# Performance work log

Hardware: AMD Instinct MI355X
Metric: run time of the kernel (lower is better)

## Reference

```python
import jax, jax.numpy as jnp
import numpy as np

N = 100000
E = 1600000
C_IN = 64
C_OUT = 64
EPS = 1e-12  # torch F.normalize default eps


def setup_inputs() -> dict:
    key = jax.random.key(0)
    k1, k2, k3, k4 = jax.random.split(key, 4)
    x = jax.random.normal(k1, (N, C_IN), dtype=jnp.float32)
    edge_index = jax.random.randint(k2, (2, E), 0, N, dtype=jnp.int64)
    # Linear(2*in_channels -> out_channels): W [out, 2*in], b [out]
    W = jax.random.normal(k3, (C_OUT, 2 * C_IN), dtype=jnp.float32) * (1.0 / np.sqrt(2 * C_IN))
    b = jax.random.normal(k4, (C_OUT,), dtype=jnp.float32) * 0.01
    return {"x": x, "edge_index": edge_index, "W": W, "b": b, "num_nodes": N}


def reference(x, edge_index, W, b, num_nodes):
    src = edge_index[0]
    dst = edge_index[1]
    # gather messages from source nodes, mean-aggregate per destination (CSC semantics)
    msg = x[src]                                   # [E, C_in]
    agg = jax.ops.segment_sum(msg, dst, num_segments=num_nodes)          # [N, C_in]
    deg = jax.ops.segment_sum(jnp.ones((msg.shape[0],), dtype=x.dtype), dst,
                              num_segments=num_nodes)                    # [N]
    agg = agg / jnp.maximum(deg, 1.0)[:, None]     # mean; zero-degree nodes -> 0
    # SAGEConvAgg output layout: concat([aggregated, root]) -> [N, 2*C_in]
    h = jnp.concatenate([agg, x], axis=-1)
    out = h @ W.T + b                              # [N, C_out]
    # l2 normalize (F.normalize, p=2, dim=-1)
    norm = jnp.sqrt(jnp.sum(out * out, axis=-1, keepdims=True))
    out = out / jnp.maximum(norm, EPS)
    return out
```

## Files before the change

### kernel.cpp

```cpp
#include <hip/hip_runtime.h>
#include <math.h>

#define CIN 64
#define NB_MAX 1024
#define CAP 2560
#define EPB 4096
#define B1T 256

__device__ __forceinline__ float rdlane_f(float v, int l) {
    return __uint_as_float(__builtin_amdgcn_readlane(__float_as_uint(v), l));
}
__device__ __forceinline__ int rdlane_i(int v, int l) {
    return (int)__builtin_amdgcn_readlane((unsigned)v, l);
}

__global__ __launch_bounds__(B1T) void build_kernel(const int* __restrict__ src,
                                                    const int* __restrict__ dst,
                                                    int* __restrict__ gcur,
                                                    int* __restrict__ coarse,
                                                    int E, int NB) {
    __shared__ int hist[NB_MAX];
    __shared__ int base[NB_MAX];
    __shared__ int cur[NB_MAX];
    const int t = threadIdx.x;
    for (int i = t; i < NB; i += B1T) { hist[i] = 0; cur[i] = 0; }
    __syncthreads();
    const int e0 = blockIdx.x * EPB;
#pragma unroll
    for (int k = 0; k < EPB / B1T; ++k) {
        int e = e0 + t + k * B1T;
        if (e < E) atomicAdd(&hist[((unsigned)dst[e]) >> 7], 1);
    }
    __syncthreads();
    for (int i = t; i < NB; i += B1T)
        base[i] = hist[i] ? atomicAdd(&gcur[i], hist[i]) : 0;
    __syncthreads();
#pragma unroll
    for (int k = 0; k < EPB / B1T; ++k) {
        int e = e0 + t + k * B1T;
        if (e < E) {
            int d  = dst[e];
            int bk = ((unsigned)d) >> 7;
            int pos = base[bk] + atomicAdd(&cur[bk], 1);
            if (pos < CAP)
                coarse[(size_t)bk * CAP + pos] = ((d & 127) << 17) | src[e];
        }
    }
}

__global__ __launch_bounds__(256) void csr_kernel(const int* __restrict__ gcur,
                                                  int* __restrict__ coarse,
                                                  int2* __restrict__ meta, int N) {
    __shared__ int pk[CAP];
    __shared__ int cnt[128], off[128], cur[128];
    const int t = threadIdx.x;
    const int bkt = blockIdx.x;
    const int m0 = gcur[bkt];
    const int m = (m0 < CAP) ? m0 : CAP;

    for (int i = t; i < m; i += 256) pk[i] = coarse[(size_t)bkt * CAP + i];
    if (t < 128) { cnt[t] = 0; cur[t] = 0; }
    __syncthreads();

    for (int i = t; i < m; i += 256) atomicAdd(&cnt[((unsigned)pk[i]) >> 17], 1);
    __syncthreads();

    int v = 0;
    if (t < 128) { v = cnt[t]; off[t] = v; }
    __syncthreads();
    for (int d = 1; d < 128; d <<= 1) {
        int add = 0;
        if (t < 128 && t >= d) add = off[t - d];
        __syncthreads();
        if (t < 128) off[t] += add;
        __syncthreads();
    }
    if (t < 128) off[t] -= v;
    __syncthreads();

    for (int i = t; i < m; i += 256) {
        int p = pk[i];
        int d = ((unsigned)p) >> 17;
        int pos = atomicAdd(&cur[d], 1);
        coarse[(size_t)bkt * CAP + off[d] + pos] = p & 0x1FFFF;
    }
    if (t < 128) {
        int n = bkt * 128 + t;
        if (n < N) meta[n] = make_int2(bkt * CAP + off[t], cnt[t]);
    }
}

__global__ __launch_bounds__(256) void gather_mean_kernel(
        const float* __restrict__ x, const int2* __restrict__ meta,
        const int* __restrict__ csr, float* __restrict__ agg, int N) {
    const int lane = threadIdx.x & 63;
    const int half = lane >> 5;
    const int c2   = lane & 31;

    const int wid = blockIdx.x * 4 + (threadIdx.x >> 6);
    const int nw  = gridDim.x * 4;

    for (int n = wid; n < N; n += nw) {
        const int2 mt = meta[n];
        const int o   = __builtin_amdgcn_readfirstlane(mt.x);
        const int deg = __builtin_amdgcn_readfirstlane(mt.y);
        const int md  = (deg < 64) ? deg : 64;

        int sv = (lane < md) ? csr[o + lane] : 0;

        float2 p0 = make_float2(0.f, 0.f), p1 = make_float2(0.f, 0.f);
        float2 p2 = make_float2(0.f, 0.f), p3 = make_float2(0.f, 0.f);
        int j = 0;
        for (; j + 8 <= md; j += 8) {
            int sA0 = rdlane_i(sv, j + 0), sB0 = rdlane_i(sv, j + 1);
            int sA1 = rdlane_i(sv, j + 2), sB1 = rdlane_i(sv, j + 3);
            int sA2 = rdlane_i(sv, j + 4), sB2 = rdlane_i(sv, j + 5);
            int sA3 = rdlane_i(sv, j + 6), sB3 = rdlane_i(sv, j + 7);
            int s0 = half ? sB0 : sA0;
            int s1 = half ? sB1 : sA1;
            int s2 = half ? sB2 : sA2;
            int s3 = half ? sB3 : sA3;
            const float2 v0 = *(const float2*)(x + ((size_t)s0 << 6) + (c2 << 1));
            const float2 v1 = *(const float2*)(x + ((size_t)s1 << 6) + (c2 << 1));
            const float2 v2 = *(const float2*)(x + ((size_t)s2 << 6) + (c2 << 1));
            const float2 v3 = *(const float2*)(x + ((size_t)s3 << 6) + (c2 << 1));
            p0.x += v0.x; p0.y += v0.y;
            p1.x += v1.x; p1.y += v1.y;
            p2.x += v2.x; p2.y += v2.y;
            p3.x += v3.x; p3.y += v3.y;
        }
        for (; j + 2 <= md; j += 2) {
            int sA = rdlane_i(sv, j), sB = rdlane_i(sv, j + 1);
            int s = half ? sB : sA;
            const float2 v = *(const float2*)(x + ((size_t)s << 6) + (c2 << 1));
            p0.x += v.x; p0.y += v.y;
        }
        if (j < md) {
            int s = rdlane_i(sv, j);
            if (half == 0) {
                const float2 v = *(const float2*)(x + ((size_t)s << 6) + (c2 << 1));
                p0.x += v.x; p0.y += v.y;
            }
        }
        float hx = (p0.x + p1.x) + (p2.x + p3.x);
        float hy = (p0.y + p1.y) + (p2.y + p3.y);
        hx += __shfl_xor(hx, 32, 64);
        hy += __shfl_xor(hy, 32, 64);
        const float inv = 1.0f / fmaxf((float)deg, 1.0f);
        if (half == 0)
            *(float2*)(agg + ((size_t)n << 6) + (c2 << 1)) =
                make_float2(hx * inv, hy * inv);
    }
}

__global__ __launch_bounds__(256) void linear_norm_kernel(
        const float* __restrict__ x, const float* __restrict__ agg,
        const float* __restrict__ W, const float* __restrict__ b,
        float* __restrict__ out, int N) {
    const int lane = threadIdx.x & 63;
    const int c2   = lane & 31;
    const float bias = b[lane];

    const int wid = blockIdx.x * 4 + (threadIdx.x >> 6);
    const int nw  = gridDim.x * 4;

    for (int n = wid; n < N; n += nw) {
        const float2 h  = *(const float2*)(agg + ((size_t)n << 6) + (c2 << 1));
        const float root = x[((size_t)n << 6) + lane];

        float c0 = bias, c1 = 0.f, c2a = 0.f, c3a = 0.f;
#pragma unroll
        for (int q = 0; q < 16; ++q) {
            const float4 wq = *(const float4*)(W + lane * 2 * CIN + q * 4);
            c0  = fmaf(rdlane_f(h.x, 2 * q),     wq.x, c0);
            c1  = fmaf(rdlane_f(h.y, 2 * q),     wq.y, c1);
            c2a = fmaf(rdlane_f(h.x, 2 * q + 1), wq.z, c2a);
            c3a = fmaf(rdlane_f(h.y, 2 * q + 1), wq.w, c3a);
        }
#pragma unroll
        for (int q = 0; q < 16; ++q) {
            const float4 wq = *(const float4*)(W + lane * 2 * CIN + CIN + q * 4);
            c0  = fmaf(rdlane_f(root, 4 * q + 0), wq.x, c0);
            c1  = fmaf(rdlane_f(root, 4 * q + 1), wq.y, c1);
            c2a = fmaf(rdlane_f(root, 4 * q + 2), wq.z, c2a);
            c3a = fmaf(rdlane_f(root, 4 * q + 3), wq.w, c3a);
        }
        float acc = (c0 + c1) + (c2a + c3a);

        float sq = acc * acc;
#pragma unroll
        for (int offs = 32; offs > 0; offs >>= 1)
            sq += __shfl_xor(sq, offs, 64);
        out[(size_t)n * CIN + lane] = acc / fmaxf(sqrtf(sq), 1e-12f);
    }
}

extern "C" void kernel_launch(void* const* d_in, const int* in_sizes, int n_in,
                              void* d_out, int out_size, void* d_ws, size_t ws_size,
                              hipStream_t stream) {
    const float* x  = (const float*)d_in[0];
    const int*   ei = (const int*)d_in[1];
    const float* W  = (const float*)d_in[2];
    const float* b  = (const float*)d_in[3];

    const int N = in_sizes[0] / CIN;
    const int E = in_sizes[1] / 2;
    const int* src = ei;
    const int* dst = ei + E;

    const int NB = (N + 127) >> 7;

    int2*  meta   = (int2*)d_ws;
    int*   gcur   = (int*)(meta + ((N + 1) & ~1));
    int*   coarse = gcur + NB_MAX;
    float* agg    = (float*)(coarse + (size_t)NB_MAX * CAP);

    hipMemsetAsync(gcur, 0, (size_t)NB * sizeof(int), stream);

    const int blocks1 = (E + EPB - 1) / EPB;
    build_kernel<<<blocks1, B1T, 0, stream>>>(src, dst, gcur, coarse, E, NB);

    csr_kernel<<<NB, 256, 0, stream>>>(gcur, coarse, meta, N);

    gather_mean_kernel<<<4096, 256, 0, stream>>>(x, meta, coarse, agg, N);

    linear_norm_kernel<<<2048, 256, 0, stream>>>(x, agg, W, b,
                                                 (float*)d_out, N);
}
```

Baseline: 261.8 us.

## Keep W rows in registers and broadcast node features through LDS

The linear+normalize kernel now loads each lane's full 128-element W row into registers once, instead of reloading it from memory for every node. Per-node agg and x values are staged in a per-wave LDS buffer and read back as float4 broadcasts, replacing the readlane broadcasts. The next node's features are prefetched while the current one is computed. The grid shrinks to 512 blocks with launch_bounds(256,2) to fit the large register footprint, which limits occupancy.

```diff
diff --git a/kernel.cpp b/kernel.cpp
--- a/kernel.cpp
+++ b/kernel.cpp
@@ -153,45 +153,61 @@
     }
 }
 
-__global__ __launch_bounds__(256) void linear_norm_kernel(
+__global__ __launch_bounds__(256, 2) void linear_norm_kernel(
         const float* __restrict__ x, const float* __restrict__ agg,
         const float* __restrict__ W, const float* __restrict__ b,
         float* __restrict__ out, int N) {
+    __shared__ __align__(16) float hbuf[4][128];
     const int lane = threadIdx.x & 63;
-    const int c2   = lane & 31;
+    const int wv   = threadIdx.x >> 6;
     const float bias = b[lane];
 
-    const int wid = blockIdx.x * 4 + (threadIdx.x >> 6);
+    float4 w[32];
+#pragma unroll
+    for (int q = 0; q < 32; ++q)
+        w[q] = *(const float4*)(W + lane * 2 * CIN + q * 4);
+#pragma unroll
+    for (int q = 0; q < 32; ++q)
+        asm volatile("" : "+v"(w[q].x), "+v"(w[q].y), "+v"(w[q].z), "+v"(w[q].w));
+
+    const int wid = blockIdx.x * 4 + wv;
     const int nw  = gridDim.x * 4;
-
-    for (int n = wid; n < N; n += nw) {
-        const float2 h  = *(const float2*)(agg + ((size_t)n << 6) + (c2 << 1));
-        const float root = x[((size_t)n << 6) + lane];
-
-        float c0 = bias, c1 = 0.f, c2a = 0.f, c3a = 0.f;
-#pragma unroll
-        for (int q = 0; q < 16; ++q) {
-            const float4 wq = *(const float4*)(W + lane * 2 * CIN + q * 4);
-            c0  = fmaf(rdlane_f(h.x, 2 * q),     wq.x, c0);
-            c1  = fmaf(rdlane_f(h.y, 2 * q),     wq.y, c1);
-            c2a = fmaf(rdlane_f(h.x, 2 * q + 1), wq.z, c2a);
-            c3a = fmaf(rdlane_f(h.y, 2 * q + 1), wq.w, c3a);
-        }
-#pragma unroll
-        for (int q = 0; q < 16; ++q) {
-            const float4 wq = *(const float4*)(W + lane * 2 * CIN + CIN + q * 4);
-            c0  = fmaf(rdlane_f(root, 4 * q + 0), wq.x, c0);
-            c1  = fmaf(rdlane_f(root, 4 * q + 1), wq.y, c1);
-            c2a = fmaf(rdlane_f(root, 4 * q + 2), wq.z, c2a);
-            c3a = fmaf(rdlane_f(root, 4 * q + 3), wq.w, c3a);
-        }
-        float acc = (c0 + c1) + (c2a + c3a);
+    const float4* hb = (const float4*)hbuf[wv];
+
+    int n = wid;
+    float av = 0.f, xv = 0.f;
+    if (n < N) {
+        av = agg[((size_t)n << 6) + lane];
+        xv = x[((size_t)n << 6) + lane];
+    }
+    for (; n < N; n += nw) {
+        hbuf[wv][lane]      = av;
+        hbuf[wv][64 + lane] = xv;
+        const int n2 = n + nw;
+        if (n2 < N) {
+            av = agg[((size_t)n2 << 6) + lane];
+            xv = x[((size_t)n2 << 6) + lane];
+        }
+        __builtin_amdgcn_wave_barrier();
+
+        float c0 = bias, c1 = 0.f, c2v = 0.f, c3v = 0.f;
+#pragma unroll
+        for (int q = 0; q < 32; ++q) {
+            const float4 hq = hb[q];
+            c0  = fmaf(hq.x, w[q].x, c0);
+            c1  = fmaf(hq.y, w[q].y, c1);
+            c2v = fmaf(hq.z, w[q].z, c2v);
+            c3v = fmaf(hq.w, w[q].w, c3v);
+        }
+        float acc = (c0 + c1) + (c2v + c3v);
 
         float sq = acc * acc;
 #pragma unroll
         for (int offs = 32; offs > 0; offs >>= 1)
             sq += __shfl_xor(sq, offs, 64);
         out[(size_t)n * CIN + lane] = acc / fmaxf(sqrtf(sq), 1e-12f);
+
+        __builtin_amdgcn_wave_barrier();
     }
 }
 
@@ -224,6 +240,6 @@
 
     gather_mean_kernel<<<4096, 256, 0, stream>>>(x, meta, coarse, agg, N);
 
-    linear_norm_kernel<<<2048, 256, 0, stream>>>(x, agg, W, b,
-                                                 (float*)d_out, N);
-}
+    linear_norm_kernel<<<512, 256, 0, stream>>>(x, agg, W, b,
+                                                (float*)d_out, N);
+}
```

New measurement: 251.8 us. -3.8%, faster.

## Restructure linear+normalize kernel to per-thread nodes with W staged in LDS

Applied to the files above, without the earlier changes.

The linear/normalize kernel now assigns two nodes per thread and accumulates all 64 outputs in registers, reading W from shared memory via broadcast. This replaces the per-wave readlane-based matvec and the cross-lane reduction for the norm. The aim is fewer cross-lane ops and better FMA density. The cost is very high register use, one block per CU, and strided per-thread global loads of agg and x rows.

```diff
diff --git a/kernel.cpp b/kernel.cpp
--- a/kernel.cpp
+++ b/kernel.cpp
@@ -153,45 +153,123 @@
     }
 }
 
-__global__ __launch_bounds__(256) void linear_norm_kernel(
+__global__ __launch_bounds__(256, 1) void linear_norm_kernel(
         const float* __restrict__ x, const float* __restrict__ agg,
         const float* __restrict__ W, const float* __restrict__ b,
         float* __restrict__ out, int N) {
+    __shared__ __align__(16) float w_lds[64 * 128 + 64];
+
+    {
+        const float4* Wv = (const float4*)W;
+        float4* w4s = (float4*)w_lds;
+        for (int i = threadIdx.x; i < 2048; i += 256) w4s[i] = Wv[i];
+        if (threadIdx.x < 16)
+            ((float4*)(w_lds + 8192))[threadIdx.x] = ((const float4*)b)[threadIdx.x];
+    }
+    __syncthreads();
+
     const int lane = threadIdx.x & 63;
-    const int c2   = lane & 31;
-    const float bias = b[lane];
-
-    const int wid = blockIdx.x * 4 + (threadIdx.x >> 6);
-    const int nw  = gridDim.x * 4;
-
-    for (int n = wid; n < N; n += nw) {
-        const float2 h  = *(const float2*)(agg + ((size_t)n << 6) + (c2 << 1));
-        const float root = x[((size_t)n << 6) + lane];
-
-        float c0 = bias, c1 = 0.f, c2a = 0.f, c3a = 0.f;
+    const int wv   = threadIdx.x >> 6;
+    const int n0   = (blockIdx.x * 4 + wv) * 128;
+    const int nA   = n0 + lane;
+    const int nB   = n0 + 64 + lane;
+    const int nAs  = (nA < N) ? nA : (N - 1);
+    const int nBs  = (nB < N) ? nB : (N - 1);
+
+    const float4* w4 = (const float4*)w_lds;
+    const float4* b4 = (const float4*)(w_lds + 8192);
+    const float4* ha = (const float4*)agg;
+    const float4* hx = (const float4*)x;
+
+    float accA[64], accB[64];
+#pragma unroll
+    for (int q = 0; q < 16; ++q) {
+        const float4 bq = b4[q];
+        accA[4 * q + 0] = bq.x; accB[4 * q + 0] = bq.x;
+        accA[4 * q + 1] = bq.y; accB[4 * q + 1] = bq.y;
+        accA[4 * q + 2] = bq.z; accB[4 * q + 2] = bq.z;
+        accA[4 * q + 3] = bq.w; accB[4 * q + 3] = bq.w;
+    }
+
+    float4 hA = ha[((size_t)nAs << 4)];
+    float4 hB = ha[((size_t)nBs << 4)];
+    for (int kq = 0; kq < 16; ++kq) {
+        const float4 cA = hA, cB = hB;
+        if (kq < 15) {
+            hA = ha[((size_t)nAs << 4) + kq + 1];
+            hB = ha[((size_t)nBs << 4) + kq + 1];
+        } else {
+            hA = hx[((size_t)nAs << 4)];
+            hB = hx[((size_t)nBs << 4)];
+        }
+#pragma unroll
+        for (int oc = 0; oc < 64; ++oc) {
+            const float4 wq = w4[oc * 32 + kq];
+            accA[oc] = fmaf(cA.w, wq.w, fmaf(cA.z, wq.z,
+                       fmaf(cA.y, wq.y, fmaf(cA.x, wq.x, accA[oc]))));
+            accB[oc] = fmaf(cB.w, wq.w, fmaf(cB.z, wq.z,
+                       fmaf(cB.y, wq.y, fmaf(cB.x, wq.x, accB[oc]))));
+        }
+    }
+    for (int kq = 0; kq < 16; ++kq) {
+        const float4 cA = hA, cB = hB;
+        if (kq < 15) {
+            hA = hx[((size_t)nAs << 4) + kq + 1];
+            hB = hx[((size_t)nBs << 4) + kq + 1];
+        }
+#pragma unroll
+        for (int oc = 0; oc < 64; ++oc) {
+            const float4 wq = w4[oc * 32 + 16 + kq];
+            accA[oc] = fmaf(cA.w, wq.w, fmaf(cA.z, wq.z,
+                       fmaf(cA.y, wq.y, fmaf(cA.x, wq.x, accA[oc]))));
+            accB[oc] = fmaf(cB.w, wq.w, fmaf(cB.z, wq.z,
+                       fmaf(cB.y, wq.y, fmaf(cB.x, wq.x, accB[oc]))));
+        }
+    }
+
+    {
+        float s0 = 0.f, s1 = 0.f, s2 = 0.f, s3 = 0.f;
 #pragma unroll
         for (int q = 0; q < 16; ++q) {
-            const float4 wq = *(const float4*)(W + lane * 2 * CIN + q * 4);
-            c0  = fmaf(rdlane_f(h.x, 2 * q),     wq.x, c0);
-            c1  = fmaf(rdlane_f(h.y, 2 * q),     wq.y, c1);
-            c2a = fmaf(rdlane_f(h.x, 2 * q + 1), wq.z, c2a);
-            c3a = fmaf(rdlane_f(h.y, 2 * q + 1), wq.w, c3a);
-        }
+            s0 = fmaf(accA[4 * q + 0], accA[4 * q + 0], s0);
+            s1 = fmaf(accA[4 * q + 1], accA[4 * q + 1], s1);
+            s2 = fmaf(accA[4 * q + 2], accA[4 * q + 2], s2);
+            s3 = fmaf(accA[4 * q + 3], accA[4 * q + 3], s3);
+        }
+        const float iA = 1.0f / fmaxf(sqrtf((s0 + s1) + (s2 + s3)), 1e-12f);
+        if (nA < N) {
+#pragma unroll
+            for (int q = 0; q < 16; ++q) {
+                float4 o;
+                o.x = accA[4 * q + 0] * iA;
+                o.y = accA[4 * q + 1] * iA;
+                o.z = accA[4 * q + 2] * iA;
+                o.w = accA[4 * q + 3] * iA;
+                *(float4*)(out + ((size_t)nA << 6) + 4 * q) = o;
+            }
+        }
+    }
+    {
+        float s0 = 0.f, s1 = 0.f, s2 = 0.f, s3 = 0.f;
 #pragma unroll
         for (int q = 0; q < 16; ++q) {
-            const float4 wq = *(const float4*)(W + lane * 2 * CIN + CIN + q * 4);
-            c0  = fmaf(rdlane_f(root, 4 * q + 0), wq.x, c0);
-            c1  = fmaf(rdlane_f(root, 4 * q + 1), wq.y, c1);
-            c2a = fmaf(rdlane_f(root, 4 * q + 2), wq.z, c2a);
-            c3a = fmaf(rdlane_f(root, 4 * q + 3), wq.w, c3a);
-        }
-        float acc = (c0 + c1) + (c2a + c3a);
-
-        float sq = acc * acc;
-#pragma unroll
-        for (int offs = 32; offs > 0; offs >>= 1)
-            sq += __shfl_xor(sq, offs, 64);
-        out[(size_t)n * CIN + lane] = acc / fmaxf(sqrtf(sq), 1e-12f);
+            s0 = fmaf(accB[4 * q + 0], accB[4 * q + 0], s0);
+            s1 = fmaf(accB[4 * q + 1], accB[4 * q + 1], s1);
+            s2 = fmaf(accB[4 * q + 2], accB[4 * q + 2], s2);
+            s3 = fmaf(accB[4 * q + 3], accB[4 * q + 3], s3);
+        }
+        const float iB = 1.0f / fmaxf(sqrtf((s0 + s1) + (s2 + s3)), 1e-12f);
+        if (nB < N) {
+#pragma unroll
+            for (int q = 0; q < 16; ++q) {
+                float4 o;
+                o.x = accB[4 * q + 0] * iB;
+                o.y = accB[4 * q + 1] * iB;
+                o.z = accB[4 * q + 2] * iB;
+                o.w = accB[4 * q + 3] * iB;
+                *(float4*)(out + ((size_t)nB << 6) + 4 * q) = o;
+            }
+        }
     }
 }
 
@@ -224,6 +302,7 @@
 
     gather_mean_kernel<<<4096, 256, 0, stream>>>(x, meta, coarse, agg, N);
 
-    linear_norm_kernel<<<2048, 256, 0, stream>>>(x, agg, W, b,
-                                                 (float*)d_out, N);
-}
+    const int blocks3b = (N + 511) / 512;
+    linear_norm_kernel<<<blocks3b, 256, 0, stream>>>(x, agg, W, b,
+                                                     (float*)d_out, N);
+}
```

Result: no change. 260.0 us (-0.7%).

## Stage W in LDS and process four nodes per wave in linear-norm kernel

Applied to the files above, without the earlier changes.

The linear+normalize kernel now copies the 32 KB weight matrix into shared memory once per block, laid out as float4 per output channel and chunk. Each wave computes four nodes at a time, so every weight load is reused across four nodes instead of being re-read from global memory per node. The grid is halved to 1024 blocks. This raises register pressure (16 accumulators plus 8 inputs) and adds a per-block LDS fill, but cuts global and L2 weight traffic per node.

```diff
diff --git a/kernel.cpp b/kernel.cpp
--- a/kernel.cpp
+++ b/kernel.cpp
@@ -157,41 +157,107 @@
         const float* __restrict__ x, const float* __restrict__ agg,
         const float* __restrict__ W, const float* __restrict__ b,
         float* __restrict__ out, int N) {
+    __shared__ __align__(16) float4 w4[2048];
+
+    for (int i = threadIdx.x; i < 2048; i += 256) {
+        const int oc = i & 63, q = i >> 6;
+        w4[i] = *(const float4*)(W + oc * 2 * CIN + q * 4);
+    }
+    __syncthreads();
+
     const int lane = threadIdx.x & 63;
-    const int c2   = lane & 31;
     const float bias = b[lane];
 
     const int wid = blockIdx.x * 4 + (threadIdx.x >> 6);
     const int nw  = gridDim.x * 4;
 
-    for (int n = wid; n < N; n += nw) {
-        const float2 h  = *(const float2*)(agg + ((size_t)n << 6) + (c2 << 1));
-        const float root = x[((size_t)n << 6) + lane];
-
-        float c0 = bias, c1 = 0.f, c2a = 0.f, c3a = 0.f;
+    for (int n0 = wid * 4; n0 < N; n0 += nw * 4) {
+        const int n1 = n0 + 1, n2 = n0 + 2, n3 = n0 + 3;
+        const bool g1 = n1 < N, g2 = n2 < N, g3 = n3 < N;
+
+        float av0 = agg[((size_t)n0 << 6) + lane];
+        float av1 = g1 ? agg[((size_t)n1 << 6) + lane] : 0.f;
+        float av2 = g2 ? agg[((size_t)n2 << 6) + lane] : 0.f;
+        float av3 = g3 ? agg[((size_t)n3 << 6) + lane] : 0.f;
+        float rv0 = x[((size_t)n0 << 6) + lane];
+        float rv1 = g1 ? x[((size_t)n1 << 6) + lane] : 0.f;
+        float rv2 = g2 ? x[((size_t)n2 << 6) + lane] : 0.f;
+        float rv3 = g3 ? x[((size_t)n3 << 6) + lane] : 0.f;
+
+        float a00 = bias, a01 = 0.f, a02 = 0.f, a03 = 0.f;
+        float a10 = bias, a11 = 0.f, a12 = 0.f, a13 = 0.f;
+        float a20 = bias, a21 = 0.f, a22 = 0.f, a23 = 0.f;
+        float a30 = bias, a31 = 0.f, a32 = 0.f, a33 = 0.f;
+
 #pragma unroll
         for (int q = 0; q < 16; ++q) {
-            const float4 wq = *(const float4*)(W + lane * 2 * CIN + q * 4);
-            c0  = fmaf(rdlane_f(h.x, 2 * q),     wq.x, c0);
-            c1  = fmaf(rdlane_f(h.y, 2 * q),     wq.y, c1);
-            c2a = fmaf(rdlane_f(h.x, 2 * q + 1), wq.z, c2a);
-            c3a = fmaf(rdlane_f(h.y, 2 * q + 1), wq.w, c3a);
+            const float4 wq = w4[q * 64 + lane];
+            a00 = fmaf(rdlane_f(av0, 4 * q + 0), wq.x, a00);
+            a01 = fmaf(rdlane_f(av0, 4 * q + 1), wq.y, a01);
+            a02 = fmaf(rdlane_f(av0, 4 * q + 2), wq.z, a02);
+            a03 = fmaf(rdlane_f(av0, 4 * q + 3), wq.w, a03);
+            a10 = fmaf(rdlane_f(av1, 4 * q + 0), wq.x, a10);
+            a11 = fmaf(rdlane_f(av1, 4 * q + 1), wq.y, a11);
+            a12 = fmaf(rdlane_f(av1, 4 * q + 2), wq.z, a12);
+            a13 = fmaf(rdlane_f(av1, 4 * q + 3), wq.w, a13);
+            a20 = fmaf(rdlane_f(av2, 4 * q + 0), wq.x, a20);
+            a21 = fmaf(rdlane_f(av2, 4 * q + 1), wq.y, a21);
+            a22 = fmaf(rdlane_f(av2, 4 * q + 2), wq.z, a22);
+            a23 = fmaf(rdlane_f(av2, 4 * q + 3), wq.w, a23);
+            a30 = fmaf(rdlane_f(av3, 4 * q + 0), wq.x, a30);
+            a31 = fmaf(rdlane_f(av3, 4 * q + 1), wq.y, a31);
+            a32 = fmaf(rdlane_f(av3, 4 * q + 2), wq.z, a32);
+            a33 = fmaf(rdlane_f(av3, 4 * q + 3), wq.w, a33);
         }
 #pragma unroll
         for (int q = 0; q < 16; ++q) {
-            const float4 wq = *(const float4*)(W + lane * 2 * CIN + CIN + q * 4);
-            c0  = fmaf(rdlane_f(root, 4 * q + 0), wq.x, c0);
-            c1  = fmaf(rdlane_f(root, 4 * q + 1), wq.y, c1);
-            c2a = fmaf(rdlane_f(root, 4 * q + 2), wq.z, c2a);
-            c3a = fmaf(rdlane_f(root, 4 * q + 3), wq.w, c3a);
-        }
-        float acc = (c0 + c1) + (c2a + c3a);
-
-        float sq = acc * acc;
-#pragma unroll
-        for (int offs = 32; offs > 0; offs >>= 1)
-            sq += __shfl_xor(sq, offs, 64);
-        out[(size_t)n * CIN + lane] = acc / fmaxf(sqrtf(sq), 1e-12f);
+            const float4 wq = w4[(16 + q) * 64 + lane];
+            a00 = fmaf(rdlane_f(rv0, 4 * q + 0), wq.x, a00);
+            a01 = fmaf(rdlane_f(rv0, 4 * q + 1), wq.y, a01);
+            a02 = fmaf(rdlane_f(rv0, 4 * q + 2), wq.z, a02);
+            a03 = fmaf(rdlane_f(rv0, 4 * q + 3), wq.w, a03);
+            a10 = fmaf(rdlane_f(rv1, 4 * q + 0), wq.x, a10);
+            a11 = fmaf(rdlane_f(rv1, 4 * q + 1), wq.y, a11);
+            a12 = fmaf(rdlane_f(rv1, 4 * q + 2), wq.z, a12);
+            a13 = fmaf(rdlane_f(rv1, 4 * q + 3), wq.w, a13);
+            a20 = fmaf(rdlane_f(rv2, 4 * q + 0), wq.x, a20);
+            a21 = fmaf(rdlane_f(rv2, 4 * q + 1), wq.y, a21);
+            a22 = fmaf(rdlane_f(rv2, 4 * q + 2), wq.z, a22);
+            a23 = fmaf(rdlane_f(rv2, 4 * q + 3), wq.w, a23);
+            a30 = fmaf(rdlane_f(rv3, 4 * q + 0), wq.x, a30);
+            a31 = fmaf(rdlane_f(rv3, 4 * q + 1), wq.y, a31);
+            a32 = fmaf(rdlane_f(rv3, 4 * q + 2), wq.z, a32);
+            a33 = fmaf(rdlane_f(rv3, 4 * q + 3), wq.w, a33);
+        }
+
+        {
+            float acc = (a00 + a01) + (a02 + a03);
+            float sq = acc * acc;
+#pragma unroll
+            for (int offs = 32; offs > 0; offs >>= 1) sq += __shfl_xor(sq, offs, 64);
+            out[(size_t)n0 * CIN + lane] = acc / fmaxf(sqrtf(sq), 1e-12f);
+        }
+        if (g1) {
+            float acc = (a10 + a11) + (a12 + a13);
+            float sq = acc * acc;
+#pragma unroll
+            for (int offs = 32; offs > 0; offs >>= 1) sq += __shfl_xor(sq, offs, 64);
+            out[(size_t)n1 * CIN + lane] = acc / fmaxf(sqrtf(sq), 1e-12f);
+        }
+        if (g2) {
+            float acc = (a20 + a21) + (a22 + a23);
+            float sq = acc * acc;
+#pragma unroll
+            for (int offs = 32; offs > 0; offs >>= 1) sq += __shfl_xor(sq, offs, 64);
+            out[(size_t)n2 * CIN + lane] = acc / fmaxf(sqrtf(sq), 1e-12f);
+        }
+        if (g3) {
+            float acc = (a30 + a31) + (a32 + a33);
+            float sq = acc * acc;
+#pragma unroll
+            for (int offs = 32; offs > 0; offs >>= 1) sq += __shfl_xor(sq, offs, 64);
+            out[(size_t)n3 * CIN + lane] = acc / fmaxf(sqrtf(sq), 1e-12f);
+        }
     }
 }
 
@@ -224,6 +290,6 @@
 
     gather_mean_kernel<<<4096, 256, 0, stream>>>(x, meta, coarse, agg, N);
 
-    linear_norm_kernel<<<2048, 256, 0, stream>>>(x, agg, W, b,
+    linear_norm_kernel<<<1024, 256, 0, stream>>>(x, agg, W, b,
                                                  (float*)d_out, N);
 }
```

After: 326.7 us. 1.25x slower.
